# Kernel tuning notes

Measured on AMD Instinct MI355X. Metric: run time of the kernel, lower is better.

## Reference

```python
import jax, jax.numpy as jnp
import numpy as np
from jax import lax

B, T, H, M, K, Q, P = 32, 128, 256, 1000, 3, 4, 2  # batch, phones, hidden, max_mel_len, kernel, q_out, p_out


def _ln(x, g, b, eps=1e-5):
    mu = jnp.mean(x, -1, keepdims=True)
    var = jnp.mean((x - mu) ** 2, -1, keepdims=True)
    return (x - mu) * lax.rsqrt(var + eps) * g + b


def _forward(x, x_mask, x_dur, params):
    (proj_w, proj_b, conv_w, conv_b, conv_g, conv_beta,
     q_w1, q_b1, q_g, q_beta, q_w2, q_b2,
     p_w1, p_b1, p_g, p_beta, p_w2, p_b2,
     proj1_w, proj1_b, proj2_w, proj2_b, projo_w, projo_b) = params

    valid = (~x_mask).astype(x.dtype)[:, :, None]                      # (B,T,1), 1 = real phone
    # proj -> ConvBlock (shared between the w and c branches; dropout is identity in eval)
    h = x @ proj_w + proj_b                                            # (B,T,H)
    hc = lax.conv_general_dilated((h * valid).transpose(0, 2, 1), conv_w,
                                  (1,), 'SAME',
                                  dimension_numbers=('NCH', 'OIH', 'NCH'))
    hc = hc.transpose(0, 2, 1) + conv_b                                # (B,T,8)
    hc = jax.nn.silu(_ln(hc, conv_g, conv_beta)) * valid               # (B,T,8)

    mel_lens = jnp.minimum(jnp.round(jnp.sum(x_dur, -1)).astype(jnp.int32), M)
    mel_pad = jnp.arange(M)[None, :] >= mel_lens[:, None]              # (B,M) True = padded frame
    mask = x_mask[:, None, :] | mel_pad[:, :, None]                    # (B,M,T)

    e = jnp.cumsum(x_dur, -1)                                          # phone end times
    s = e - x_dur                                                      # phone start times
    t = jnp.arange(1, M + 1, dtype=x.dtype)
    E = jnp.where(mask, 0.0, e[:, None, :] - t[None, :, None])         # (B,M,T)
    S = jnp.where(mask, 0.0, t[None, :, None] - s[:, None, :])         # (B,M,T)

    feat = jnp.concatenate([jnp.broadcast_to(hc[:, None], (B, M, T, 8)),
                            S[..., None], E[..., None]], axis=-1)      # (B,M,T,10)

    # mlp_q scores -> masked softmax over phone axis
    sc = jax.nn.silu(_ln(feat @ q_w1 + q_b1, q_g, q_beta)) @ q_w2 + q_b2   # (B,M,T,Q)
    sc = jnp.where(x_mask[:, None, :, None], -jnp.inf, sc)
    w = jax.nn.softmax(sc, axis=2)
    w = jnp.where(mel_pad[:, :, None, None], 0.0, w)                   # (B,M,T,Q)

    # mlp_p per-(frame,phone) auxiliary features
    c = jax.nn.silu(_ln(feat @ p_w1 + p_b1, p_g, p_beta)) @ p_w2 + p_b2    # (B,M,T,P)

    # dual einsum combine (matches torch permute+view ordering: q-major then feature)
    wh = jnp.einsum('bmnq,bnh->bmqh', w, x).reshape(B, M, Q * H) @ proj1_w + proj1_b
    wc = jnp.einsum('bmnq,bmnp->bmqp', w, c).reshape(B, M, Q * P) @ proj2_w + proj2_b
    o = jnp.where(mel_pad[:, :, None], 0.0, wh + wc) @ projo_w + projo_b   # (B,M,2H)

    mel_mask = jnp.broadcast_to(mel_pad[:, :, None], (B, M, T))
    return o, mel_mask, mel_lens, jnp.transpose(w, (0, 3, 1, 2))


def setup_inputs() -> dict:
    key = jax.random.key(0)
    ks = jax.random.split(key, 16)
    x = jax.random.normal(ks[0], (B, T, H), jnp.float32)
    x_lengths = jax.random.randint(ks[1], (B,), T // 2, T + 1).at[0].set(T)
    x_mask = jnp.arange(T)[None, :] >= x_lengths[:, None]              # True = pad
    x_dur = jax.random.uniform(ks[2], (B, T), jnp.float32, 2.0, 10.0)
    x_dur = x_dur * (~x_mask)
    x_dur = x_dur.at[0].multiply(2.0)  # element 0 total duration > M -> static max_mel_len = M

    def xavier(k, shape):
        return jax.random.normal(k, shape, jnp.float32) * jnp.sqrt(2.0 / (shape[0] + shape[1]))

    return dict(
        x=x, x_mask=x_mask, x_dur=x_dur, x_lengths=x_lengths,
        proj_w=xavier(ks[3], (H, H)), proj_b=jnp.zeros((H,)),
        conv_w=jax.random.normal(ks[4], (8, H, K), jnp.float32) * 0.05, conv_b=jnp.zeros((8,)),
        conv_g=jnp.ones((8,)), conv_beta=jnp.zeros((8,)),
        q_w1=xavier(ks[5], (10, Q)), q_b1=jnp.zeros((Q,)),
        q_g=jnp.ones((Q,)), q_beta=jnp.zeros((Q,)),
        q_w2=xavier(ks[6], (Q, Q)), q_b2=jnp.zeros((Q,)),
        p_w1=xavier(ks[7], (10, P)), p_b1=jnp.zeros((P,)),
        p_g=jnp.ones((P,)), p_beta=jnp.zeros((P,)),
        p_w2=xavier(ks[8], (P, P)), p_b2=jnp.zeros((P,)),
        proj1_w=xavier(ks[9], (H * Q, H)), proj1_b=jnp.zeros((H,)),
        proj2_w=xavier(ks[10], (Q * P, H)), proj2_b=jnp.zeros((H,)),
        projo_w=xavier(ks[11], (H, 2 * H)), projo_b=jnp.zeros((2 * H,)),
    )


def reference(x, x_mask, x_dur, x_lengths,
              proj_w, proj_b, conv_w, conv_b, conv_g, conv_beta,
              q_w1, q_b1, q_g, q_beta, q_w2, q_b2,
              p_w1, p_b1, p_g, p_beta, p_w2, p_b2,
              proj1_w, proj1_b, proj2_w, proj2_b, projo_w, projo_b):
    params = (proj_w, proj_b, conv_w, conv_b, conv_g, conv_beta,
              q_w1, q_b1, q_g, q_beta, q_w2, q_b2,
              p_w1, p_b1, p_g, p_beta, p_w2, p_b2,
              proj1_w, proj1_b, proj2_w, proj2_b, projo_w, projo_b)
    return _forward(x, x_mask, x_dur, params)
```

## Files before the change

### kernel.cpp

```cpp
#include <hip/hip_runtime.h>
#include <math.h>

#define BB 32
#define TT 128
#define HH 256
#define MM 1000

typedef __attribute__((ext_vector_type(8))) short short8;
typedef __attribute__((ext_vector_type(4))) float floatx4;

__device__ inline void fma4(float4& a, const float4 b, float s) {
    a.x += b.x * s; a.y += b.y * s; a.z += b.z * s; a.w += b.w * s;
}

__device__ inline unsigned short f2bf(float f) {
    union { float f; unsigned int u; } c; c.f = f;
    unsigned int u = c.u;
    return (unsigned short)((u + 0x7FFFu + ((u >> 16) & 1u)) >> 16);
}

__device__ inline float bf2f(unsigned short h) {
    union { unsigned int u; float f; } c; c.u = ((unsigned int)h) << 16; return c.f;
}


__global__ void k_prep(const float* __restrict__ dur, float* __restrict__ e_cum,
                       int* __restrict__ ml_i, float* __restrict__ ml_out) {
    int b = blockIdx.x;
    if (threadIdx.x == 0) {
        float run = 0.f;
        const float* d = dur + b * TT;
        float* e = e_cum + b * TT;
        for (int t = 0; t < TT; ++t) { run += d[t]; e[t] = run; }
        int ml = (int)rintf(run);
        if (ml > MM) ml = MM;
        if (ml < 0) ml = 0;
        ml_i[b] = ml;
        ml_out[b] = (float)ml;
    }
}

__global__ __launch_bounds__(256) void k_h(const float* __restrict__ x,
                                           const float* __restrict__ pw,
                                           const float* __restrict__ pb,
                                           float* __restrict__ h) {
    __shared__ float xs[16][HH];
    int blk = blockIdx.x;
    int b = blk >> 3, tt = blk & 7;
    int t0 = tt * 16;
    int tid = threadIdx.x;
    for (int e = tid; e < 16 * HH; e += 256) {
        int r = e >> 8, i = e & 255;
        xs[r][i] = x[(b * TT + t0 + r) * HH + i];
    }
    __syncthreads();
    int jg = tid & 63, rg = tid >> 6;
    int j4 = jg * 4;
    float4 bias = *(const float4*)(pb + j4);
    float4 acc[4];
    #pragma unroll
    for (int ri = 0; ri < 4; ++ri) acc[ri] = bias;
    #pragma unroll 4
    for (int i = 0; i < HH; ++i) {
        float4 wv = *(const float4*)(pw + i * HH + j4);
        #pragma unroll
        for (int ri = 0; ri < 4; ++ri) fma4(acc[ri], wv, xs[rg * 4 + ri][i]);
    }
    #pragma unroll
    for (int ri = 0; ri < 4; ++ri)
        *(float4*)(h + (b * TT + t0 + rg * 4 + ri) * HH + j4) = acc[ri];
}

__global__ __launch_bounds__(128) void k_conv(const float* __restrict__ h,
                                              const float* __restrict__ cw,
                                              const int* __restrict__ xlen,
                                              float* __restrict__ hcpre) {
    __shared__ float hs[18][257];
    __shared__ float cws[8][769];
    int blk = blockIdx.x;
    int b = blk >> 3, tt = blk & 7;
    int t0 = tt * 16;
    int tid = threadIdx.x;
    int L = xlen[b];
    for (int e = tid; e < 18 * 256; e += 128) {
        int r = e >> 8, i = e & 255;
        int t = t0 - 1 + r;
        float v = 0.f;
        if (t >= 0 && t < TT && t < L) v = h[((size_t)b * TT + t) * HH + i];
        hs[r][i] = v;
    }
    for (int e = tid; e < 6144; e += 128) {
        int o = e / 768, rem = e - o * 768;
        cws[o][rem] = cw[e];
    }
    __syncthreads();
    int o = tid >> 4, tl = tid & 15;
    float acc = 0.f;
    #pragma unroll
    for (int k = 0; k < 3; ++k) {
        const float* wr = &cws[o][k];
        const float* hr = hs[tl + k];
        #pragma unroll 8
        for (int i = 0; i < 256; ++i) acc += hr[i] * wr[i * 3];
    }
    hcpre[((size_t)b * TT + t0 + tl) * 8 + o] = acc;
}

__global__ __launch_bounds__(128) void k_bases(
    const float* __restrict__ hcpre, const float* __restrict__ cb,
    const float* __restrict__ cg, const float* __restrict__ cbeta,
    const float* __restrict__ qw1, const float* __restrict__ qb1,
    const float* __restrict__ pw1, const float* __restrict__ pb1,
    const float* __restrict__ e_cum, const float* __restrict__ dur,
    const int* __restrict__ xlen,
    float* __restrict__ baseq, float* __restrict__ basep) {
    int b = blockIdx.x;
    int t = threadIdx.x;
    int L = xlen[b];
    float v[8];
    float mu = 0.f;
    #pragma unroll
    for (int o = 0; o < 8; ++o) { v[o] = hcpre[(b * TT + t) * 8 + o] + cb[o]; mu += v[o]; }
    mu *= 0.125f;
    float var = 0.f;
    #pragma unroll
    for (int o = 0; o < 8; ++o) { float d = v[o] - mu; var += d * d; }
    var *= 0.125f;
    float rs = 1.0f / sqrtf(var + 1e-5f);
    float valid = (t < L) ? 1.f : 0.f;
    #pragma unroll
    for (int o = 0; o < 8; ++o) {
        float a = (v[o] - mu) * rs * cg[o] + cbeta[o];
        v[o] = a / (1.f + expf(-a)) * valid;
    }
    float e = e_cum[b * TT + t];
    float s_ = e - dur[b * TT + t];
    #pragma unroll
    for (int j = 0; j < 4; ++j) {
        float acc = qb1[j];
        #pragma unroll
        for (int o = 0; o < 8; ++o) acc += v[o] * qw1[o * 4 + j];
        acc += e * qw1[9 * 4 + j] - s_ * qw1[8 * 4 + j];
        baseq[(b * TT + t) * 4 + j] = acc;
    }
    #pragma unroll
    for (int j = 0; j < 2; ++j) {
        float acc = pb1[j];
        #pragma unroll
        for (int o = 0; o < 8; ++o) acc += v[o] * pw1[o * 2 + j];
        acc += e * pw1[9 * 2 + j] - s_ * pw1[8 * 2 + j];
        basep[(b * TT + t) * 2 + j] = acc;
    }
}

__global__ __launch_bounds__(256) void k_wsoft(
    const float* __restrict__ baseq, const float* __restrict__ basep,
    const float* __restrict__ qw1, const float* __restrict__ qg,
    const float* __restrict__ qbeta, const float* __restrict__ qw2,
    const float* __restrict__ qb2,
    const float* __restrict__ pw1, const float* __restrict__ pg,
    const float* __restrict__ pbeta, const float* __restrict__ pw2,
    const float* __restrict__ pb2,
    const int* __restrict__ xlen, const int* __restrict__ ml_i,
    float* __restrict__ w_out, float* __restrict__ mm_out,
    float* __restrict__ wc8) {
    int blk = blockIdx.x;
    int b = blk / 250;
    int mg = blk - b * 250;
    int wv = threadIdx.x >> 6, lane = threadIdx.x & 63;
    int m = mg * 4 + wv;
    int ml = ml_i[b];
    int t1 = lane, t2 = lane + 64;
    bool pad = (m >= ml);
    size_t mmbase = ((size_t)b * MM + m) * TT;
    mm_out[mmbase + t1] = pad ? 1.f : 0.f;
    mm_out[mmbase + t2] = pad ? 1.f : 0.f;
    if (pad) {
        #pragma unroll
        for (int q = 0; q < 4; ++q) {
            size_t wb = ((size_t)(b * 4 + q) * MM + m) * TT;
            w_out[wb + t1] = 0.f;
            w_out[wb + t2] = 0.f;
        }
        if (lane == 0) {
            #pragma unroll
            for (int r = 0; r < 8; ++r) wc8[((size_t)b * MM + m) * 8 + r] = 0.f;
        }
        return;
    }
    int L = xlen[b];
    float mp1 = (float)(m + 1);
    float dq[4];
    #pragma unroll
    for (int j = 0; j < 4; ++j) dq[j] = mp1 * (qw1[8 * 4 + j] - qw1[9 * 4 + j]);

    float sc1[4], sc2[4];
    float c1v[2], c2v[2];
    #pragma unroll
    for (int half = 0; half < 2; ++half) {
        int t = half ? t2 : t1;
        float* sc = half ? sc2 : sc1;
        float* cv = half ? c2v : c1v;
        if (t < L) {
            float4 bq = *(const float4*)(baseq + ((size_t)b * TT + t) * 4);
            float z[4] = {bq.x + dq[0], bq.y + dq[1], bq.z + dq[2], bq.w + dq[3]};
            float mu = 0.25f * (z[0] + z[1] + z[2] + z[3]);
            float var = 0.f;
            #pragma unroll
            for (int j = 0; j < 4; ++j) { float d = z[j] - mu; var += d * d; }
            var *= 0.25f;
            float rs = 1.f / sqrtf(var + 1e-5f);
            float a[4];
            #pragma unroll
            for (int j = 0; j < 4; ++j) {
                float av = (z[j] - mu) * rs * qg[j] + qbeta[j];
                a[j] = av / (1.f + expf(-av));
            }
            #pragma unroll
            for (int q = 0; q < 4; ++q) {
                float s = qb2[q];
                #pragma unroll
                for (int j = 0; j < 4; ++j) s += a[j] * qw2[j * 4 + q];
                sc[q] = s;
            }
            float z0 = basep[((size_t)b * TT + t) * 2 + 0] + mp1 * (pw1[16] - pw1[18]);
            float z1 = basep[((size_t)b * TT + t) * 2 + 1] + mp1 * (pw1[17] - pw1[19]);
            float pmu = 0.5f * (z0 + z1);
            float d0 = z0 - pmu, d1 = z1 - pmu;
            float pvar = 0.5f * (d0 * d0 + d1 * d1);
            float prs = 1.f / sqrtf(pvar + 1e-5f);
            float a0 = d0 * prs * pg[0] + pbeta[0];
            float a1 = d1 * prs * pg[1] + pbeta[1];
            a0 = a0 / (1.f + expf(-a0));
            a1 = a1 / (1.f + expf(-a1));
            cv[0] = pb2[0] + a0 * pw2[0] + a1 * pw2[2];
            cv[1] = pb2[1] + a0 * pw2[1] + a1 * pw2[3];
        } else {
            sc[0] = sc[1] = sc[2] = sc[3] = -__builtin_inff();
            cv[0] = cv[1] = 0.f;
        }
    }
    float w1[4], w2[4];
    #pragma unroll
    for (int q = 0; q < 4; ++q) {
        float mx = fmaxf(sc1[q], sc2[q]);
        #pragma unroll
        for (int off = 32; off > 0; off >>= 1) mx = fmaxf(mx, __shfl_xor(mx, off, 64));
        float e1 = expf(sc1[q] - mx);
        float e2 = expf(sc2[q] - mx);
        float s = e1 + e2;
        #pragma unroll
        for (int off = 32; off > 0; off >>= 1) s += __shfl_xor(s, off, 64);
        w1[q] = e1 / s;
        w2[q] = e2 / s;
        size_t wb = ((size_t)(b * 4 + q) * MM + m) * TT;
        w_out[wb + t1] = w1[q];
        w_out[wb + t2] = w2[q];
    }
    float red[8];
    #pragma unroll
    for (int r8 = 0; r8 < 8; ++r8) {
        int q = r8 >> 1, p = r8 & 1;
        float v = w1[q] * c1v[p] + w2[q] * c2v[p];
        #pragma unroll
        for (int off = 32; off > 0; off >>= 1) v += __shfl_xor(v, off, 64);
        red[r8] = v;
    }
    if (lane == 0) {
        #pragma unroll
        for (int r8 = 0; r8 < 8; ++r8) wc8[((size_t)b * MM + m) * 8 + r8] = red[r8];
    }
}

__global__ __launch_bounds__(256) void k_pw_part(const float* __restrict__ p1w,
                                                 const float* __restrict__ po,
                                                 float* __restrict__ PWpart) {
    __shared__ float S[16][64];
    int blk = blockIdx.x;
    int ks = blk & 3, colT = (blk >> 2) & 7, ht = blk >> 5;
    int q = colT >> 1, j0 = (colT & 1) * 256;
    int h0 = ht * 16, k0 = ks * 64;
    int tid = threadIdx.x;
    for (int e = tid; e < 1024; e += 256) {
        int r = e >> 6, c = e & 63;
        S[r][c] = p1w[(q * 256 + h0 + r) * 256 + k0 + c];
    }
    __syncthreads();
    int jg = tid & 63, rg = tid >> 6;
    int jcol = j0 + jg * 4;
    float4 acc[4];
    #pragma unroll
    for (int r = 0; r < 4; ++r) acc[r] = make_float4(0, 0, 0, 0);
    float4 nb = *(const float4*)(po + (size_t)k0 * 512 + jcol);
    for (int c = 0; c < 64; ++c) {
        float4 cur = nb;
        if (c < 63) nb = *(const float4*)(po + (size_t)(k0 + c + 1) * 512 + jcol);
        #pragma unroll
        for (int r = 0; r < 4; ++r) fma4(acc[r], cur, S[rg * 4 + r][c]);
    }
    #pragma unroll
    for (int r = 0; r < 4; ++r) {
        int hh = h0 + rg * 4 + r;
        *(float4*)(PWpart + (size_t)ks * 524288 + hh * 2048 + q * 512 + jcol) = acc[r];
    }
}

__global__ __launch_bounds__(256) void k_pwt(const float* __restrict__ PWpart,
                                             unsigned short* __restrict__ pwh,
                                             unsigned short* __restrict__ pwl) {
    __shared__ float S[64][65];
    int blk = blockIdx.x;
    int nt = blk & 31, ct = blk >> 5;
    int c0 = ct * 64, n0 = nt * 64;
    int tid = threadIdx.x;
    for (int e = tid; e < 4096; e += 256) {
        int cc = e >> 6, nn = e & 63;
        size_t off = (size_t)(c0 + cc) * 2048 + n0 + nn;
        float v = PWpart[off] + PWpart[524288 + off]
                + PWpart[2 * 524288 + off] + PWpart[3 * 524288 + off];
        S[cc][nn] = v;
    }
    __syncthreads();
    for (int e = tid; e < 4096; e += 256) {
        int nn = e >> 6, cc = e & 63;
        float v = S[cc][nn];
        unsigned short h = f2bf(v);
        size_t d = (size_t)(n0 + nn) * 256 + c0 + cc;
        pwh[d] = h;
        pwl[d] = f2bf(v - bf2f(h));
    }
}

__global__ __launch_bounds__(256) void k_xcvt(const float* __restrict__ x,
                                              unsigned short* __restrict__ xh,
                                              unsigned short* __restrict__ xl) {
    int idx = (blockIdx.x * 256 + threadIdx.x) * 4;
    float4 v = *(const float4*)(x + idx);
    float vv[4] = {v.x, v.y, v.z, v.w};
    union { unsigned short us[4]; uint2 u; } hi, lo;
    #pragma unroll
    for (int k = 0; k < 4; ++k) {
        unsigned short h = f2bf(vv[k]);
        hi.us[k] = h;
        lo.us[k] = f2bf(vv[k] - bf2f(h));
    }
    *(uint2*)(xh + idx) = hi.u;
    *(uint2*)(xl + idx) = lo.u;
}

__global__ __launch_bounds__(512) void k_small(const float* __restrict__ p2w,
    const float* __restrict__ po, const float* __restrict__ p1b,
    const float* __restrict__ p2b, const float* __restrict__ pob,
    float* __restrict__ P2o, float* __restrict__ bvec) {
    int j = threadIdx.x;
    float acc[9];
    #pragma unroll
    for (int r = 0; r < 9; ++r) acc[r] = 0.f;
    for (int c = 0; c < HH; ++c) {
        float pv = po[c * 512 + j];
        #pragma unroll
        for (int r = 0; r < 8; ++r) acc[r] += p2w[r * HH + c] * pv;
        acc[8] += (p1b[c] + p2b[c]) * pv;
    }
    #pragma unroll
    for (int r = 0; r < 8; ++r) P2o[r * 512 + j] = acc[r];
    bvec[j] = acc[8] + pob[j];
}

__device__ inline int swzk(int row, int chunk) {
    return row * 32 + ((chunk ^ ((row >> 1) & 3)) << 3);
}

__global__ __launch_bounds__(256) void k_A2m(const unsigned short* __restrict__ xh,
                                             const unsigned short* __restrict__ xl,
                                             const unsigned short* __restrict__ pwh,
                                             const unsigned short* __restrict__ pwl,
                                             unsigned short* __restrict__ A2T) {
    __shared__ __align__(16) unsigned short SM[16384];
    unsigned short* Ah = SM;
    unsigned short* Al = SM + 4096;
    unsigned short* Bh = SM + 8192;
    unsigned short* Bl = SM + 12288;
    int blk = blockIdx.x;
    int b = blk >> 4, nt = blk & 15;
    int n0 = nt * 128;
    int tid = threadIdx.x;
    int lane = tid & 63, wv = tid >> 6;
    int wm = wv & 1, wn = wv >> 1;

    floatx4 acc[16];
    #pragma unroll
    for (int i = 0; i < 16; ++i) acc[i] = (floatx4){0.f, 0.f, 0.f, 0.f};

    int srow = tid >> 1, shalf = tid & 1;
    const unsigned short* gxh = xh + ((size_t)(b * TT + srow) * 256 + shalf * 16);
    const unsigned short* gxl = xl + ((size_t)(b * TT + srow) * 256 + shalf * 16);
    const unsigned short* gph = pwh + ((size_t)(n0 + srow) * 256 + shalf * 16);
    const unsigned short* gpl = pwl + ((size_t)(n0 + srow) * 256 + shalf * 16);
    int wAd0 = swzk(srow, 2 * shalf);
    int wAd1 = swzk(srow, 2 * shalf + 1);

    int ra = wm * 64 + (lane & 15);
    int rb = wn * 64 + (lane & 15);
    int cq = lane >> 4;

    for (int kc = 0; kc < 256; kc += 32) {
        uint4 a0 = *(const uint4*)(gxh + kc);
        uint4 a1 = *(const uint4*)(gxh + kc + 8);
        uint4 a2 = *(const uint4*)(gxl + kc);
        uint4 a3 = *(const uint4*)(gxl + kc + 8);
        uint4 b0 = *(const uint4*)(gph + kc);
        uint4 b1 = *(const uint4*)(gph + kc + 8);
        uint4 b2 = *(const uint4*)(gpl + kc);
        uint4 b3 = *(const uint4*)(gpl + kc + 8);
        *(uint4*)&Ah[wAd0] = a0; *(uint4*)&Ah[wAd1] = a1;
        *(uint4*)&Al[wAd0] = a2; *(uint4*)&Al[wAd1] = a3;
        *(uint4*)&Bh[wAd0] = b0; *(uint4*)&Bh[wAd1] = b1;
        *(uint4*)&Bl[wAd0] = b2; *(uint4*)&Bl[wAd1] = b3;
        __syncthreads();
        short8 afh[4], afl[4], bfh[4], bfl[4];
        #pragma unroll
        for (int i = 0; i < 4; ++i) {
            afh[i] = *(const short8*)&Ah[swzk(ra + i * 16, cq)];
            afl[i] = *(const short8*)&Al[swzk(ra + i * 16, cq)];
            bfh[i] = *(const short8*)&Bh[swzk(rb + i * 16, cq)];
            bfl[i] = *(const short8*)&Bl[swzk(rb + i * 16, cq)];
        }
        #pragma unroll
        for (int i = 0; i < 4; ++i)
            #pragma unroll
            for (int j = 0; j < 4; ++j) {
                floatx4 c = acc[i * 4 + j];
                c = __builtin_amdgcn_mfma_f32_16x16x32_bf16(afh[i], bfh[j], c, 0, 0, 0);
                c = __builtin_amdgcn_mfma_f32_16x16x32_bf16(afh[i], bfl[j], c, 0, 0, 0);
                c = __builtin_amdgcn_mfma_f32_16x16x32_bf16(afl[i], bfh[j], c, 0, 0, 0);
                acc[i * 4 + j] = c;
            }
        __syncthreads();
    }

    unsigned short* OT = SM;
    #pragma unroll
    for (int i = 0; i < 4; ++i)
        #pragma unroll
        for (int j = 0; j < 4; ++j) {
            int nloc = wn * 64 + j * 16 + (lane & 15);
            int tb = wm * 64 + i * 16 + ((lane >> 4) << 2);
            union { unsigned short us[4]; uint2 v; } pk;
            #pragma unroll
            for (int r = 0; r < 4; ++r) pk.us[r] = f2bf(acc[i * 4 + j][r]);
            int chunk = tb >> 3, sub = tb & 7;
            *(uint2*)&OT[nloc * 128 + (((chunk ^ (nloc & 15)) << 3) | sub)] = pk.v;
        }
    __syncthreads();
    int q = n0 >> 9, jb = n0 & 511;
    for (int u = tid; u < 2048; u += 256) {
        int nrow = u >> 4, seg = u & 15;
        uint4 v = *(const uint4*)&OT[nrow * 128 + ((seg ^ (nrow & 15)) << 3)];
        *(uint4*)(A2T + ((size_t)(b * 512 + jb + nrow)) * 512 + q * 128 + seg * 8) = v;
    }
}

__global__ __launch_bounds__(256) void k_main(
    const float* __restrict__ w_out, const unsigned short* __restrict__ A2T,
    const float* __restrict__ wc8, const float* __restrict__ P2o,
    const float* __restrict__ bvec, const float* __restrict__ pob,
    const int* __restrict__ ml_i, float* __restrict__ o_out) {
    __shared__ __align__(16) unsigned short Asm[128 * 40];
    __shared__ __align__(16) unsigned short Bsm[128 * 40];
    int blk = blockIdx.x;
    int nt = blk & 3, mt = (blk >> 2) & 7, b = blk >> 5;
    int m0 = mt * 128, n0 = nt * 128;
    int tid = threadIdx.x;
    int lane = tid & 63, wv = tid >> 6;
    int wm = wv & 1, wn = wv >> 1;

    floatx4 acc[16];
    #pragma unroll
    for (int i = 0; i < 16; ++i) acc[i] = (floatx4){0.f, 0.f, 0.f, 0.f};

    int srow = tid >> 1, shalf = tid & 1;
    int arow_base = wm * 64 + (lane & 15);
    int brow_base = wn * 64 + (lane & 15);
    int acol = (lane >> 4) * 8;

    for (int kc = 0; kc < 512; kc += 32) {
        int q = kc >> 7, tk = kc & 127;
        {
            int m = m0 + srow;
            union { unsigned short us[16]; uint4 q4[2]; } pk;
            if (m < MM) {
                const float* src = w_out + ((size_t)(b * 4 + q) * MM + m) * TT + tk + shalf * 16;
                #pragma unroll
                for (int g = 0; g < 4; ++g) {
                    float4 v = ((const float4*)src)[g];
                    pk.us[g * 4 + 0] = f2bf(v.x); pk.us[g * 4 + 1] = f2bf(v.y);
                    pk.us[g * 4 + 2] = f2bf(v.z); pk.us[g * 4 + 3] = f2bf(v.w);
                }
            } else {
                pk.q4[0] = make_uint4(0, 0, 0, 0);
                pk.q4[1] = make_uint4(0, 0, 0, 0);
            }
            *(uint4*)(&Asm[srow * 40 + shalf * 16]) = pk.q4[0];
            *(uint4*)(&Asm[srow * 40 + shalf * 16 + 8]) = pk.q4[1];
        }
        {
            const unsigned short* srcB = A2T + ((size_t)b * 512 + n0 + srow) * 512 + kc + shalf * 16;
            uint4 v0 = *(const uint4*)srcB;
            uint4 v1 = *(const uint4*)(srcB + 8);
            *(uint4*)(&Bsm[srow * 40 + shalf * 16]) = v0;
            *(uint4*)(&Bsm[srow * 40 + shalf * 16 + 8]) = v1;
        }
        __syncthreads();
        short8 af[4], bfr[4];
        #pragma unroll
        for (int i = 0; i < 4; ++i)
            af[i] = *(const short8*)(&Asm[(arow_base + i * 16) * 40 + acol]);
        #pragma unroll
        for (int j = 0; j < 4; ++j)
            bfr[j] = *(const short8*)(&Bsm[(brow_base + j * 16) * 40 + acol]);
        #pragma unroll
        for (int i = 0; i < 4; ++i)
            #pragma unroll
            for (int j = 0; j < 4; ++j)
                acc[i * 4 + j] = __builtin_amdgcn_mfma_f32_16x16x32_bf16(
                    af[i], bfr[j], acc[i * 4 + j], 0, 0, 0);
        __syncthreads();
    }

    float* wc8s = (float*)Asm;
    float* P2os = (float*)Bsm;
    float* bvs  = (float*)Bsm + 1024;
    float* pobs = (float*)Bsm + 1152;
    for (int e = tid; e < 1024; e += 256) {
        int mm_ = e >> 3, r = e & 7;
        int m = m0 + mm_;
        wc8s[e] = (m < MM) ? wc8[((size_t)b * MM + m) * 8 + r] : 0.f;
    }
    for (int e = tid; e < 1024; e += 256) {
        int r = e >> 7, j = e & 127;
        P2os[e] = P2o[r * 512 + n0 + j];
    }
    if (tid < 128) {
        bvs[tid] = bvec[n0 + tid];
        pobs[tid] = pob[n0 + tid];
    }
    __syncthreads();
    int ml = ml_i[b];
    #pragma unroll
    for (int i = 0; i < 4; ++i) {
        #pragma unroll
        for (int j = 0; j < 4; ++j) {
            int nloc = wn * 64 + j * 16 + (lane & 15);
            #pragma unroll
            for (int reg = 0; reg < 4; ++reg) {
                int mloc = wm * 64 + i * 16 + (lane >> 4) * 4 + reg;
                int m = m0 + mloc;
                if (m >= MM) continue;
                float v;
                if (m < ml) {
                    v = acc[i * 4 + j][reg] + bvs[nloc];
                    #pragma unroll
                    for (int r8 = 0; r8 < 8; ++r8)
                        v += wc8s[mloc * 8 + r8] * P2os[r8 * 128 + nloc];
                } else {
                    v = pobs[nloc];
                }
                o_out[((size_t)b * MM + m) * 512 + n0 + nloc] = v;
            }
        }
    }
}

extern "C" void kernel_launch(void* const* d_in, const int* in_sizes, int n_in,
                              void* d_out, int out_size, void* d_ws, size_t ws_size,
                              hipStream_t stream) {
    (void)in_sizes; (void)n_in; (void)out_size; (void)ws_size;
    const float* x      = (const float*)d_in[0];
    const float* dur    = (const float*)d_in[2];
    const int*   xlen   = (const int*)d_in[3];
    const float* proj_w = (const float*)d_in[4];
    const float* proj_b = (const float*)d_in[5];
    const float* conv_w = (const float*)d_in[6];
    const float* conv_b = (const float*)d_in[7];
    const float* conv_g = (const float*)d_in[8];
    const float* conv_be= (const float*)d_in[9];
    const float* q_w1   = (const float*)d_in[10];
    const float* q_b1   = (const float*)d_in[11];
    const float* q_g    = (const float*)d_in[12];
    const float* q_be   = (const float*)d_in[13];
    const float* q_w2   = (const float*)d_in[14];
    const float* q_b2   = (const float*)d_in[15];
    const float* p_w1   = (const float*)d_in[16];
    const float* p_b1   = (const float*)d_in[17];
    const float* p_g    = (const float*)d_in[18];
    const float* p_be   = (const float*)d_in[19];
    const float* p_w2   = (const float*)d_in[20];
    const float* p_b2   = (const float*)d_in[21];
    const float* p1w    = (const float*)d_in[22];
    const float* p1b    = (const float*)d_in[23];
    const float* p2w    = (const float*)d_in[24];
    const float* p2b    = (const float*)d_in[25];
    const float* pow_   = (const float*)d_in[26];
    const float* pob    = (const float*)d_in[27];

    float* ws    = (float*)d_ws;
    float* e_cum = ws + 0;
    float* hcpre = ws + 4096;
    float* baseq = ws + 36864;
    float* basep = ws + 53248;
    float* h     = ws + 61440;
    unsigned short* x_hi = (unsigned short*)(ws + 61440);
    unsigned short* x_lo = (unsigned short*)(ws + 585728);
    unsigned short* pw_h = (unsigned short*)(ws + 1110016);
    unsigned short* pw_l = (unsigned short*)(ws + 1372160);
    unsigned short* A2T = (unsigned short*)(ws + 1634304);
    float* wc8   = ws + 5828608;
    float* P2o   = ws + 6084608;
    float* bvec  = ws + 6088704;
    int*   ml_i  = (int*)(ws + 6089216);
    float* PWpart= ws + 6090752;

    float* o_out  = (float*)d_out;
    float* mm_out = o_out + 16384000;
    float* ml_out = o_out + 20480000;
    float* w_out  = o_out + 20480032;

    k_prep<<<dim3(BB), dim3(64), 0, stream>>>(dur, e_cum, ml_i, ml_out);
    k_h<<<dim3(BB * 8), dim3(256), 0, stream>>>(x, proj_w, proj_b, h);
    k_conv<<<dim3(BB * 8), dim3(128), 0, stream>>>(h, conv_w, xlen, hcpre);
    k_xcvt<<<dim3(1024), dim3(256), 0, stream>>>(x, x_hi, x_lo);
    k_bases<<<dim3(BB), dim3(128), 0, stream>>>(hcpre, conv_b, conv_g, conv_be,
                                                q_w1, q_b1, p_w1, p_b1,
                                                e_cum, dur, xlen, baseq, basep);
    k_pw_part<<<dim3(512), dim3(256), 0, stream>>>(p1w, pow_, PWpart);
    k_pwt<<<dim3(128), dim3(256), 0, stream>>>(PWpart, pw_h, pw_l);
    k_small<<<dim3(1), dim3(512), 0, stream>>>(p2w, pow_, p1b, p2b, pob, P2o, bvec);
    k_A2m<<<dim3(512), dim3(256), 0, stream>>>(x_hi, x_lo, pw_h, pw_l, A2T);
    k_wsoft<<<dim3(BB * 250), dim3(256), 0, stream>>>(baseq, basep,
                                                      q_w1, q_g, q_be, q_w2, q_b2,
                                                      p_w1, p_g, p_be, p_w2, p_b2,
                                                      xlen, ml_i, w_out, mm_out, wc8);
    k_main<<<dim3(BB * 32), dim3(256), 0, stream>>>(w_out, A2T, wc8, P2o, bvec,
                                                    pob, ml_i, o_out);
}
```

Measured before the change: 433.1 us.

## Stage softmax weights as padded bf16 and load full K=128 tiles in main GEMM

k_wsoft now also writes the softmax weights as bf16 into a workspace buffer padded to 1024 rows, and k_prep zeroes the padding rows. k_main reads that bf16 buffer directly instead of re-reading the fp32 w_out and converting it per tile. k_main also loads whole 128-wide K slices per q into XOR-swizzled shared memory and runs four MFMA k-steps per barrier pair instead of one per 32-wide slice. A2T is re-laid out per q to match. This reduces global traffic and barrier count in the GEMM, at the cost of extra bf16 stores in k_wsoft and more shared memory per block, which may lower occupancy.

```diff
diff --git a/kernel.cpp b/kernel.cpp
--- a/kernel.cpp
+++ b/kernel.cpp
@@ -25,9 +25,16 @@
 
 
 __global__ void k_prep(const float* __restrict__ dur, float* __restrict__ e_cum,
-                       int* __restrict__ ml_i, float* __restrict__ ml_out) {
+                       int* __restrict__ ml_i, float* __restrict__ ml_out,
+                       unsigned short* __restrict__ w_bf) {
     int b = blockIdx.x;
-    if (threadIdx.x == 0) {
+    int tid = threadIdx.x;
+    #pragma unroll
+    for (int q = 0; q < 4; ++q) {
+        uint4* dst = (uint4*)(w_bf + (((size_t)(b * 4 + q)) * 1024 + 1000) * 128);
+        for (int e = tid; e < 384; e += 64) dst[e] = make_uint4(0, 0, 0, 0);
+    }
+    if (tid == 0) {
         float run = 0.f;
         const float* d = dur + b * TT;
         float* e = e_cum + b * TT;
@@ -163,7 +170,7 @@
     const float* __restrict__ pb2,
     const int* __restrict__ xlen, const int* __restrict__ ml_i,
     float* __restrict__ w_out, float* __restrict__ mm_out,
-    float* __restrict__ wc8) {
+    float* __restrict__ wc8, unsigned short* __restrict__ w_bf) {
     int blk = blockIdx.x;
     int b = blk / 250;
     int mg = blk - b * 250;
@@ -181,6 +188,8 @@
             size_t wb = ((size_t)(b * 4 + q) * MM + m) * TT;
             w_out[wb + t1] = 0.f;
             w_out[wb + t2] = 0.f;
+            unsigned short* wbq = w_bf + (((size_t)(b * 4 + q)) * 1024 + m) * 128;
+            wbq[t1] = 0; wbq[t2] = 0;
         }
         if (lane == 0) {
             #pragma unroll
@@ -256,6 +265,9 @@
         size_t wb = ((size_t)(b * 4 + q) * MM + m) * TT;
         w_out[wb + t1] = w1[q];
         w_out[wb + t2] = w2[q];
+        unsigned short* wbq = w_bf + (((size_t)(b * 4 + q)) * 1024 + m) * 128;
+        wbq[t1] = f2bf(w1[q]);
+        wbq[t2] = f2bf(w2[q]);
     }
     float red[8];
     #pragma unroll
@@ -457,17 +469,17 @@
     for (int u = tid; u < 2048; u += 256) {
         int nrow = u >> 4, seg = u & 15;
         uint4 v = *(const uint4*)&OT[nrow * 128 + ((seg ^ (nrow & 15)) << 3)];
-        *(uint4*)(A2T + ((size_t)(b * 512 + jb + nrow)) * 512 + q * 128 + seg * 8) = v;
+        *(uint4*)(A2T + (((size_t)(b * 4 + q) * 512) + jb + nrow) * 128 + seg * 8) = v;
     }
 }
 
 __global__ __launch_bounds__(256) void k_main(
-    const float* __restrict__ w_out, const unsigned short* __restrict__ A2T,
+    const unsigned short* __restrict__ w_bf, const unsigned short* __restrict__ A2T,
     const float* __restrict__ wc8, const float* __restrict__ P2o,
     const float* __restrict__ bvec, const float* __restrict__ pob,
     const int* __restrict__ ml_i, float* __restrict__ o_out) {
-    __shared__ __align__(16) unsigned short Asm[128 * 40];
-    __shared__ __align__(16) unsigned short Bsm[128 * 40];
+    __shared__ __align__(16) unsigned short Asm[128 * 128];
+    __shared__ __align__(16) unsigned short Bsm[128 * 128];
     int blk = blockIdx.x;
     int nt = blk & 3, mt = (blk >> 2) & 7, b = blk >> 5;
     int m0 = mt * 128, n0 = nt * 128;
@@ -479,54 +491,51 @@
     #pragma unroll
     for (int i = 0; i < 16; ++i) acc[i] = (floatx4){0.f, 0.f, 0.f, 0.f};
 
-    int srow = tid >> 1, shalf = tid & 1;
-    int arow_base = wm * 64 + (lane & 15);
-    int brow_base = wn * 64 + (lane & 15);
-    int acol = (lane >> 4) * 8;
-
-    for (int kc = 0; kc < 512; kc += 32) {
-        int q = kc >> 7, tk = kc & 127;
-        {
-            int m = m0 + srow;
-            union { unsigned short us[16]; uint4 q4[2]; } pk;
-            if (m < MM) {
-                const float* src = w_out + ((size_t)(b * 4 + q) * MM + m) * TT + tk + shalf * 16;
+    int rl = lane >> 4;
+    int cl = lane & 15;
+    int ra = wm * 64 + cl;
+    int rb = wn * 64 + cl;
+
+    for (int q = 0; q < 4; ++q) {
+        uint4 la[8], lb[8];
+        #pragma unroll
+        for (int j = 0; j < 8; ++j) {
+            int e = tid + j * 256;
+            int row = e >> 4, chunk = e & 15;
+            la[j] = *(const uint4*)(w_bf +
+                (((size_t)(b * 4 + q)) * 1024 + m0 + row) * 128 + chunk * 8);
+            lb[j] = *(const uint4*)(A2T +
+                (((size_t)(b * 4 + q)) * 512 + n0 + row) * 128 + chunk * 8);
+        }
+        if (q) __syncthreads();
+        #pragma unroll
+        for (int j = 0; j < 8; ++j) {
+            int e = tid + j * 256;
+            int row = e >> 4, chunk = e & 15;
+            int d = row * 128 + ((chunk ^ (row & 15)) << 3);
+            *(uint4*)&Asm[d] = la[j];
+            *(uint4*)&Bsm[d] = lb[j];
+        }
+        __syncthreads();
+        #pragma unroll
+        for (int kk = 0; kk < 4; ++kk) {
+            int csw = ((kk * 4 + rl) ^ cl) << 3;
+            short8 af[4], bfr[4];
+            #pragma unroll
+            for (int i = 0; i < 4; ++i)
+                af[i] = *(const short8*)&Asm[(ra + i * 16) * 128 + csw];
+            #pragma unroll
+            for (int j2 = 0; j2 < 4; ++j2)
+                bfr[j2] = *(const short8*)&Bsm[(rb + j2 * 16) * 128 + csw];
+            #pragma unroll
+            for (int i = 0; i < 4; ++i)
                 #pragma unroll
-                for (int g = 0; g < 4; ++g) {
-                    float4 v = ((const float4*)src)[g];
-                    pk.us[g * 4 + 0] = f2bf(v.x); pk.us[g * 4 + 1] = f2bf(v.y);
-                    pk.us[g * 4 + 2] = f2bf(v.z); pk.us[g * 4 + 3] = f2bf(v.w);
-                }
-            } else {
-                pk.q4[0] = make_uint4(0, 0, 0, 0);
-                pk.q4[1] = make_uint4(0, 0, 0, 0);
-            }
-            *(uint4*)(&Asm[srow * 40 + shalf * 16]) = pk.q4[0];
-            *(uint4*)(&Asm[srow * 40 + shalf * 16 + 8]) = pk.q4[1];
-        }
-        {
-            const unsigned short* srcB = A2T + ((size_t)b * 512 + n0 + srow) * 512 + kc + shalf * 16;
-            uint4 v0 = *(const uint4*)srcB;
-            uint4 v1 = *(const uint4*)(srcB + 8);
-            *(uint4*)(&Bsm[srow * 40 + shalf * 16]) = v0;
-            *(uint4*)(&Bsm[srow * 40 + shalf * 16 + 8]) = v1;
-        }
-        __syncthreads();
-        short8 af[4], bfr[4];
-        #pragma unroll
-        for (int i = 0; i < 4; ++i)
-            af[i] = *(const short8*)(&Asm[(arow_base + i * 16) * 40 + acol]);
-        #pragma unroll
-        for (int j = 0; j < 4; ++j)
-            bfr[j] = *(const short8*)(&Bsm[(brow_base + j * 16) * 40 + acol]);
-        #pragma unroll
-        for (int i = 0; i < 4; ++i)
-            #pragma unroll
-            for (int j = 0; j < 4; ++j)
-                acc[i * 4 + j] = __builtin_amdgcn_mfma_f32_16x16x32_bf16(
-                    af[i], bfr[j], acc[i * 4 + j], 0, 0, 0);
-        __syncthreads();
-    }
+                for (int j2 = 0; j2 < 4; ++j2)
+                    acc[i * 4 + j2] = __builtin_amdgcn_mfma_f32_16x16x32_bf16(
+                        af[i], bfr[j2], acc[i * 4 + j2], 0, 0, 0);
+        }
+    }
+    __syncthreads();
 
     float* wc8s = (float*)Asm;
     float* P2os = (float*)Bsm;
@@ -620,13 +629,14 @@
     float* bvec  = ws + 6088704;
     int*   ml_i  = (int*)(ws + 6089216);
     float* PWpart= ws + 6090752;
+    unsigned short* w_bf = (unsigned short*)(ws + 8187904);
 
     float* o_out  = (float*)d_out;
     float* mm_out = o_out + 16384000;
     float* ml_out = o_out + 20480000;
     float* w_out  = o_out + 20480032;
 
-    k_prep<<<dim3(BB), dim3(64), 0, stream>>>(dur, e_cum, ml_i, ml_out);
+    k_prep<<<dim3(BB), dim3(64), 0, stream>>>(dur, e_cum, ml_i, ml_out, w_bf);
     k_h<<<dim3(BB * 8), dim3(256), 0, stream>>>(x, proj_w, proj_b, h);
     k_conv<<<dim3(BB * 8), dim3(128), 0, stream>>>(h, conv_w, xlen, hcpre);
     k_xcvt<<<dim3(1024), dim3(256), 0, stream>>>(x, x_hi, x_lo);
@@ -640,7 +650,7 @@
     k_wsoft<<<dim3(BB * 250), dim3(256), 0, stream>>>(baseq, basep,
                                                       q_w1, q_g, q_be, q_w2, q_b2,
                                                       p_w1, p_g, p_be, p_w2, p_b2,
-                                                      xlen, ml_i, w_out, mm_out, wc8);
-    k_main<<<dim3(BB * 32), dim3(256), 0, stream>>>(w_out, A2T, wc8, P2o, bvec,
+                                                      xlen, ml_i, w_out, mm_out, wc8, w_bf);
+    k_main<<<dim3(BB * 32), dim3(256), 0, stream>>>(w_bf, A2T, wc8, P2o, bvec,
                                                     pob, ml_i, o_out);
 }
```

New measurement: 457.4 us. +5.6%, slower.
